# Performance work log

Measured on AMD Instinct MI355X. Metric: run time of the kernel, lower is better.

## Reference

```python
import jax, jax.numpy as jnp
import numpy as np

B, S, I, H = 32, 2048, 256, 256


def setup_inputs() -> dict:
    key = jax.random.key(0)
    ks = jax.random.split(key, 12)
    scale = 1.0 / np.sqrt(H + I)  # torch Linear default init scale-ish
    def w(k):
        return jax.random.normal(k, (H + I, H), dtype=jnp.float32) * scale
    def b(k):
        return jax.random.normal(k, (H,), dtype=jnp.float32) * scale
    return {
        "x": jax.random.normal(ks[0], (B, S, I), dtype=jnp.float32),
        "h0": jax.random.normal(ks[1], (1, B, H), dtype=jnp.float32),
        "c0": jax.random.normal(ks[2], (1, B, H), dtype=jnp.float32),
        "Wf": w(ks[3]), "bf": b(ks[4]),
        "Wi": w(ks[5]), "bi": b(ks[6]),
        "Wc": w(ks[7]), "bc": b(ks[8]),
        "Wo": w(ks[9]), "bo": b(ks[10]),
    }


def reference(x, h0, c0, Wf, bf, Wi, bi, Wc, bc, Wo, bo):
    # Fuse the four gate GEMMs into one: W_all [H+I, 4H], b_all [4H]
    W_all = jnp.concatenate([Wf, Wi, Wc, Wo], axis=1)
    b_all = jnp.concatenate([bf, bi, bc, bo], axis=0)
    Hh = h0.shape[-1]

    def step(carry, x_t):
        h, c = carry  # [B,H]
        hx = jnp.concatenate([h, x_t], axis=-1)          # [B, H+I]
        g = hx @ W_all + b_all                            # [B, 4H]
        f = jax.nn.sigmoid(g[:, 0*Hh:1*Hh])
        i = jax.nn.sigmoid(g[:, 1*Hh:2*Hh])
        cand = jnp.tanh(g[:, 2*Hh:3*Hh])
        o = jax.nn.sigmoid(g[:, 3*Hh:4*Hh])
        c_new = c * f + i * cand
        h_new = o * jnp.tanh(c_new)
        return (h_new, c_new), h_new

    (h_f, c_f), hs = jax.lax.scan(step, (h0[0], c0[0]), jnp.swapaxes(x, 0, 1))
    hidden_states = jnp.swapaxes(hs, 0, 1)               # [B,S,H]
    return hidden_states, (h_f[None], c_f[None])
```

## Files before the change

### kernel.cpp

```cpp
#include <hip/hip_runtime.h>
#include <hip/hip_bf16.h>

typedef __attribute__((ext_vector_type(8))) short short8;
typedef __attribute__((ext_vector_type(4))) float floatx4;
typedef __attribute__((ext_vector_type(4))) unsigned int uintx4;
typedef unsigned int u32;
typedef unsigned long long u64;

#define Bb 32
#define Ss 2048
#define Ii 256
#define Hh 256

#define TAGS_OFF 4096
#define DATA_OFF 8192
#define GX_OFF   65536

#define RETRY_LATCH (1u << 18)
#define RETRY_DEAD  (1u << 22)

__device__ __forceinline__ unsigned short f2bf(float f) {
    unsigned int u = __float_as_uint(f);
    u += 0x7fffu + ((u >> 16) & 1u);
    return (unsigned short)(u >> 16);
}
__device__ __forceinline__ float bf2f_lo(u32 w) { return __uint_as_float(w << 16); }
__device__ __forceinline__ float bf2f_hi(u32 w) { return __uint_as_float(w & 0xffff0000u); }

__device__ __forceinline__ float fast_sigmoid(float x) {
    return __builtin_amdgcn_rcpf(1.0f + __expf(-x));
}
__device__ __forceinline__ float fast_tanh(float x) {
    return 1.0f - 2.0f * __builtin_amdgcn_rcpf(__expf(2.0f * x) + 1.0f);
}

__device__ __forceinline__ void vm_drain() {
    asm volatile("s_waitcnt vmcnt(0)" ::: "memory");
}
__device__ __forceinline__ void tag_load16(const u32* pt, uintx4& a, uintx4& b, uintx4& c, uintx4& d) {
    asm volatile("global_load_dwordx4 %0, %4, off sc0 sc1\n\t"
                 "global_load_dwordx4 %1, %4, off offset:16 sc0 sc1\n\t"
                 "global_load_dwordx4 %2, %4, off offset:32 sc0 sc1\n\t"
                 "global_load_dwordx4 %3, %4, off offset:48 sc0 sc1\n\t"
                 "s_waitcnt vmcnt(0)"
                 : "=v"(a), "=v"(b), "=v"(c), "=v"(d) : "v"(pt) : "memory");
}
__device__ __forceinline__ void data_load8(const u32* pd, uintx4 v[8]) {
    asm volatile("global_load_dwordx4 %0, %8, off sc0 sc1\n\t"
                 "global_load_dwordx4 %1, %8, off offset:64 sc0 sc1\n\t"
                 "global_load_dwordx4 %2, %8, off offset:128 sc0 sc1\n\t"
                 "global_load_dwordx4 %3, %8, off offset:192 sc0 sc1\n\t"
                 "global_load_dwordx4 %4, %8, off offset:256 sc0 sc1\n\t"
                 "global_load_dwordx4 %5, %8, off offset:320 sc0 sc1\n\t"
                 "global_load_dwordx4 %6, %8, off offset:384 sc0 sc1\n\t"
                 "global_load_dwordx4 %7, %8, off offset:448 sc0 sc1\n\t"
                 "s_waitcnt vmcnt(0)"
                 : "=v"(v[0]), "=v"(v[1]), "=v"(v[2]), "=v"(v[3]),
                   "=v"(v[4]), "=v"(v[5]), "=v"(v[6]), "=v"(v[7])
                 : "v"(pd) : "memory");
}

__global__ __launch_bounds__(256, 2)
void lstm_gx_kernel(const float* __restrict__ x,
                    const float* __restrict__ Wf, const float* __restrict__ bfp,
                    const float* __restrict__ Wi, const float* __restrict__ bip,
                    const float* __restrict__ Wc, const float* __restrict__ bcp,
                    const float* __restrict__ Wo, const float* __restrict__ bop,
                    u32* __restrict__ gx)
{
    const int tid = threadIdx.x, wave = tid >> 6, lane = tid & 63;
    const int ln = lane & 15, lg = lane >> 4;
    const int combo = blockIdx.x & 7;
    const int tbase = (blockIdx.x >> 3) * 8;
    const int wg = ((combo & 1) << 2) + wave;
    const int chalf = (combo >> 1) & 1, mtile = combo >> 2;
    const int j0 = wg * 32 + chalf * 16, r0 = mtile * 16;
    const int wv = wg * 4 + chalf * 2 + mtile;

    const float* Wg[4] = {Wf, Wi, Wc, Wo};
    const float* bg[4] = {bfp, bip, bcp, bop};
    float bias[4];
#pragma unroll
    for (int g = 0; g < 4; ++g) bias[g] = bg[g][j0 + ln];

    short8 Bf[4][8];
#pragma unroll
    for (int g = 0; g < 4; ++g)
#pragma unroll
        for (int ks = 0; ks < 8; ++ks) {
            short8 v;
#pragma unroll
            for (int i = 0; i < 8; ++i) {
                int k = 256 + 32 * ks + 8 * lg + i;
                v[i] = (short)f2bf(Wg[g][k * Hh + (j0 + ln)]);
            }
            Bf[g][ks] = v;
        }

    for (int it = 0; it < 8; ++it) {
        int t = tbase + it;
        short8 xf[8];
#pragma unroll
        for (int ks = 0; ks < 8; ++ks) {
            const float* px = x + (r0 + ln) * (Ss * Ii) + t * Ii + 32 * ks + 8 * lg;
            floatx4 a = *(const floatx4*)px;
            floatx4 b = *(const floatx4*)(px + 4);
            short8 v;
#pragma unroll
            for (int q = 0; q < 4; ++q) { v[q] = (short)f2bf(a[q]); v[4 + q] = (short)f2bf(b[q]); }
            xf[ks] = v;
        }
        floatx4 acc[4];
#pragma unroll
        for (int g = 0; g < 4; ++g) acc[g] = (floatx4){0.f, 0.f, 0.f, 0.f};
#pragma unroll
        for (int ks = 0; ks < 8; ++ks)
#pragma unroll
            for (int g = 0; g < 4; ++g)
                acc[g] = __builtin_amdgcn_mfma_f32_16x16x32_bf16(xf[ks], Bf[g][ks], acc[g], 0, 0, 0);

        u32 o[8];
#pragma unroll
        for (int g = 0; g < 4; ++g)
#pragma unroll
            for (int rp = 0; rp < 2; ++rp) {
                float v0 = acc[g][2 * rp] + bias[g];
                float v1 = acc[g][2 * rp + 1] + bias[g];
                o[g * 2 + rp] = (u32)f2bf(v0) | ((u32)f2bf(v1) << 16);
            }
        u32* dst = gx + ((size_t)(t * 32 + wv) * 64 + lane) * 8;
        ((uintx4*)dst)[0] = (uintx4){o[0], o[1], o[2], o[3]};
        ((uintx4*)dst)[1] = (uintx4){o[4], o[5], o[6], o[7]};
    }
}

__global__ __launch_bounds__(256, 1)
void lstm_rec5(const float* __restrict__ h0,
               const float* __restrict__ c0,
               const float* __restrict__ Wf,
               const float* __restrict__ Wi,
               const float* __restrict__ Wc,
               const float* __restrict__ Wo,
               float* __restrict__ out,
               u32* tags, u32* data, const u32* __restrict__ gx)
{
    const int wg = blockIdx.x;
    const int tid = threadIdx.x;
    const int wave = tid >> 6, lane = tid & 63;
    const int mt = wave & 1, chalf = wave >> 1;
    const int ln = lane & 15, lg = lane >> 4;
    const int j0 = wg * 32 + chalf * 16;
    const int j = j0 + ln;
    const int wv = wg * 4 + chalf * 2 + mt;

    const float* Wg[4] = {Wf, Wi, Wc, Wo};
    short8 Bfrag[4][8];
#pragma unroll
    for (int g = 0; g < 4; ++g)
#pragma unroll
        for (int ks = 0; ks < 8; ++ks) {
            short8 v;
#pragma unroll
            for (int i = 0; i < 8; ++i) {
                int k = 32 * ks + 8 * lg + i;
                v[i] = (short)f2bf(Wg[g][k * Hh + j]);
            }
            Bfrag[g][ks] = v;
        }

    float cst[4], hl[4];
#pragma unroll
    for (int r = 0; r < 4; ++r) {
        cst[r] = c0[(16 * mt + 4 * lg + r) * Hh + j];
        hl[r] = 0.0f;
    }

    bool use_atomic = false;

    auto publish = [&](int slot, u32 tag, const float h[4]) {
        u32 wrd[4];
#pragma unroll
        for (int r = 0; r < 4; ++r) {
            float partner = __shfl_xor(h[r], 1);
            wrd[r] = (u32)f2bf(h[r]) | ((u32)f2bf(partner) << 16);
        }
        u32* pd = data + slot * 4096 + (16 * mt + 4 * lg) * 128 + (j >> 1);
        if ((ln & 1) == 0) {
#pragma unroll
            for (int r = 0; r < 4; ++r)
                __hip_atomic_store(pd + 128 * r, wrd[r], __ATOMIC_RELAXED, __HIP_MEMORY_SCOPE_AGENT);
        }
        vm_drain();
        if (lane == 0)
            __hip_atomic_store(tags + (slot * 2 + mt) * 16 + (wg * 2 + chalf), tag,
                               __ATOMIC_RELAXED, __HIP_MEMORY_SCOPE_AGENT);
    };

    {
        float hv0[4];
#pragma unroll
        for (int r = 0; r < 4; ++r) hv0[r] = h0[(16 * mt + 4 * lg + r) * Hh + j];
        publish(0, 1u, hv0);
    }

    uintx4 g0, g1;
    {
        const uintx4* p = (const uintx4*)(gx + ((size_t)wv * 64 + lane) * 8);
        g0 = p[0]; g1 = p[1];
    }

    for (int t = 0; t < Ss; ++t) {
        const int slot = t & 1;
        const u32 want = (u32)(t + 1);
        const u32* pt = tags + (slot * 2 + mt) * 16;

        {
            u32 it = 0;
            for (;;) {
                u32 bad;
                if (!use_atomic) {
                    uintx4 a, b, c, d;
                    tag_load16(pt, a, b, c, d);
                    bad = (a.x ^ want) | (a.y ^ want) | (a.z ^ want) | (a.w ^ want)
                        | (b.x ^ want) | (b.y ^ want) | (b.z ^ want) | (b.w ^ want)
                        | (c.x ^ want) | (c.y ^ want) | (c.z ^ want) | (c.w ^ want)
                        | (d.x ^ want) | (d.y ^ want) | (d.z ^ want) | (d.w ^ want);
                } else {
                    bad = 0;
#pragma unroll
                    for (int i = 0; i < 16; ++i)
                        bad |= __hip_atomic_load(pt + i, __ATOMIC_RELAXED,
                                                 __HIP_MEMORY_SCOPE_AGENT) ^ want;
                }
                if (!__any((int)(bad != 0))) break;
                ++it;
                if (it >= RETRY_LATCH) use_atomic = true;
                if (it >= RETRY_DEAD) break;
            }
        }

        uintx4 dv[8];
        const u32* pd = data + slot * 4096 + (16 * mt + ln) * 128 + 4 * lg;
        if (!use_atomic) {
            data_load8(pd, dv);
        } else {
            const u64* pq = (const u64*)pd;
#pragma unroll
            for (int ks = 0; ks < 8; ++ks) {
                u64 u0 = __hip_atomic_load(pq + 8 * ks,     __ATOMIC_RELAXED, __HIP_MEMORY_SCOPE_AGENT);
                u64 u1 = __hip_atomic_load(pq + 8 * ks + 1, __ATOMIC_RELAXED, __HIP_MEMORY_SCOPE_AGENT);
                dv[ks] = (uintx4){(u32)u0, (u32)(u0 >> 32), (u32)u1, (u32)(u1 >> 32)};
            }
        }

        floatx4 acc[4];
        acc[0] = (floatx4){bf2f_lo(g0.x), bf2f_hi(g0.x), bf2f_lo(g0.y), bf2f_hi(g0.y)};
        acc[1] = (floatx4){bf2f_lo(g0.z), bf2f_hi(g0.z), bf2f_lo(g0.w), bf2f_hi(g0.w)};
        acc[2] = (floatx4){bf2f_lo(g1.x), bf2f_hi(g1.x), bf2f_lo(g1.y), bf2f_hi(g1.y)};
        acc[3] = (floatx4){bf2f_lo(g1.z), bf2f_hi(g1.z), bf2f_lo(g1.w), bf2f_hi(g1.w)};
        if (t + 1 < Ss) {
            const uintx4* pn = (const uintx4*)(gx + ((size_t)((t + 1) * 32 + wv) * 64 + lane) * 8);
            g0 = pn[0]; g1 = pn[1];
        }

#pragma unroll
        for (int ks = 0; ks < 8; ++ks) {
            union { uintx4 u; short8 s; } cv;
            cv.u = dv[ks];
#pragma unroll
            for (int g = 0; g < 4; ++g)
                acc[g] = __builtin_amdgcn_mfma_f32_16x16x32_bf16(cv.s, Bfrag[g][ks], acc[g], 0, 0, 0);
        }

        float hnew[4];
#pragma unroll
        for (int r = 0; r < 4; ++r) {
            float fg = fast_sigmoid(acc[0][r]);
            float ig = fast_sigmoid(acc[1][r]);
            float cd = fast_tanh(acc[2][r]);
            float og = fast_sigmoid(acc[3][r]);
            float c  = cst[r] * fg + ig * cd;
            cst[r] = c;
            hnew[r] = og * fast_tanh(c);
            hl[r] = hnew[r];
        }

        publish((t + 1) & 1, (u32)(t + 2), hnew);
#pragma unroll
        for (int r = 0; r < 4; ++r)
            out[(16 * mt + 4 * lg + r) * (Ss * Hh) + t * Hh + j] = hnew[r];
    }

    float* hfo = out + Bb * Ss * Hh;
    float* cfo = hfo + Bb * Hh;
#pragma unroll
    for (int r = 0; r < 4; ++r) {
        int b = 16 * mt + 4 * lg + r;
        hfo[b * Hh + j] = hl[r];
        cfo[b * Hh + j] = cst[r];
    }
}

extern "C" void kernel_launch(void* const* d_in, const int* in_sizes, int n_in,
                              void* d_out, int out_size, void* d_ws, size_t ws_size,
                              hipStream_t stream) {
    (void)in_sizes; (void)n_in; (void)out_size; (void)ws_size;
    const float* x  = (const float*)d_in[0];
    const float* h0 = (const float*)d_in[1];
    const float* c0 = (const float*)d_in[2];
    const float* Wf = (const float*)d_in[3]; const float* bf = (const float*)d_in[4];
    const float* Wi = (const float*)d_in[5]; const float* bi = (const float*)d_in[6];
    const float* Wc = (const float*)d_in[7]; const float* bc = (const float*)d_in[8];
    const float* Wo = (const float*)d_in[9]; const float* bo = (const float*)d_in[10];

    u32* tags = (u32*)((char*)d_ws + TAGS_OFF);
    u32* data = (u32*)((char*)d_ws + DATA_OFF);
    u32* gx   = (u32*)((char*)d_ws + GX_OFF);


    hipLaunchKernelGGL(lstm_gx_kernel, dim3(2048), dim3(256), 0, stream,
                       x, Wf, bf, Wi, bi, Wc, bc, Wo, bo, gx);
    hipLaunchKernelGGL(lstm_rec5, dim3(8), dim3(256), 0, stream,
                       h0, c0, Wf, Wi, Wc, Wo, (float*)d_out, tags, data, gx);
}
```

Measured before the change: 7.365 ms.

## Replace tag-then-data handoff with self-tagged per-element ring words

```diff
diff --git a/kernel.cpp b/kernel.cpp
--- a/kernel.cpp
+++ b/kernel.cpp
@@ -5,19 +5,16 @@
 typedef __attribute__((ext_vector_type(4))) float floatx4;
 typedef __attribute__((ext_vector_type(4))) unsigned int uintx4;
 typedef unsigned int u32;
-typedef unsigned long long u64;
 
 #define Bb 32
 #define Ss 2048
 #define Ii 256
 #define Hh 256
 
-#define TAGS_OFF 4096
-#define DATA_OFF 8192
-#define GX_OFF   65536
-
-#define RETRY_LATCH (1u << 18)
-#define RETRY_DEAD  (1u << 22)
+#define RING_OFF 8192
+#define GX_OFF   131072
+
+#define RETRY_DEAD (1u << 22)
 
 __device__ __forceinline__ unsigned short f2bf(float f) {
     unsigned int u = __float_as_uint(f);
@@ -34,30 +31,30 @@
     return 1.0f - 2.0f * __builtin_amdgcn_rcpf(__expf(2.0f * x) + 1.0f);
 }
 
-__device__ __forceinline__ void vm_drain() {
-    asm volatile("s_waitcnt vmcnt(0)" ::: "memory");
-}
-__device__ __forceinline__ void tag_load16(const u32* pt, uintx4& a, uintx4& b, uintx4& c, uintx4& d) {
-    asm volatile("global_load_dwordx4 %0, %4, off sc0 sc1\n\t"
-                 "global_load_dwordx4 %1, %4, off offset:16 sc0 sc1\n\t"
-                 "global_load_dwordx4 %2, %4, off offset:32 sc0 sc1\n\t"
-                 "global_load_dwordx4 %3, %4, off offset:48 sc0 sc1\n\t"
-                 "s_waitcnt vmcnt(0)"
-                 : "=v"(a), "=v"(b), "=v"(c), "=v"(d) : "v"(pt) : "memory");
-}
-__device__ __forceinline__ void data_load8(const u32* pd, uintx4 v[8]) {
-    asm volatile("global_load_dwordx4 %0, %8, off sc0 sc1\n\t"
-                 "global_load_dwordx4 %1, %8, off offset:64 sc0 sc1\n\t"
-                 "global_load_dwordx4 %2, %8, off offset:128 sc0 sc1\n\t"
-                 "global_load_dwordx4 %3, %8, off offset:192 sc0 sc1\n\t"
-                 "global_load_dwordx4 %4, %8, off offset:256 sc0 sc1\n\t"
-                 "global_load_dwordx4 %5, %8, off offset:320 sc0 sc1\n\t"
-                 "global_load_dwordx4 %6, %8, off offset:384 sc0 sc1\n\t"
-                 "global_load_dwordx4 %7, %8, off offset:448 sc0 sc1\n\t"
-                 "s_waitcnt vmcnt(0)"
-                 : "=v"(v[0]), "=v"(v[1]), "=v"(v[2]), "=v"(v[3]),
-                   "=v"(v[4]), "=v"(v[5]), "=v"(v[6]), "=v"(v[7])
-                 : "v"(pd) : "memory");
+__device__ __forceinline__ void ring_load_all(const u32* p, uintx4 A[8], uintx4 B[8]) {
+    asm volatile(
+        "global_load_dwordx4 %0, %16, off sc0 sc1\n\t"
+        "global_load_dwordx4 %1, %16, off offset:16 sc0 sc1\n\t"
+        "global_load_dwordx4 %2, %16, off offset:128 sc0 sc1\n\t"
+        "global_load_dwordx4 %3, %16, off offset:144 sc0 sc1\n\t"
+        "global_load_dwordx4 %4, %16, off offset:256 sc0 sc1\n\t"
+        "global_load_dwordx4 %5, %16, off offset:272 sc0 sc1\n\t"
+        "global_load_dwordx4 %6, %16, off offset:384 sc0 sc1\n\t"
+        "global_load_dwordx4 %7, %16, off offset:400 sc0 sc1\n\t"
+        "global_load_dwordx4 %8, %16, off offset:512 sc0 sc1\n\t"
+        "global_load_dwordx4 %9, %16, off offset:528 sc0 sc1\n\t"
+        "global_load_dwordx4 %10, %16, off offset:640 sc0 sc1\n\t"
+        "global_load_dwordx4 %11, %16, off offset:656 sc0 sc1\n\t"
+        "global_load_dwordx4 %12, %16, off offset:768 sc0 sc1\n\t"
+        "global_load_dwordx4 %13, %16, off offset:784 sc0 sc1\n\t"
+        "global_load_dwordx4 %14, %16, off offset:896 sc0 sc1\n\t"
+        "global_load_dwordx4 %15, %16, off offset:912 sc0 sc1\n\t"
+        "s_waitcnt vmcnt(0)"
+        : "=v"(A[0]), "=v"(B[0]), "=v"(A[1]), "=v"(B[1]),
+          "=v"(A[2]), "=v"(B[2]), "=v"(A[3]), "=v"(B[3]),
+          "=v"(A[4]), "=v"(B[4]), "=v"(A[5]), "=v"(B[5]),
+          "=v"(A[6]), "=v"(B[6]), "=v"(A[7]), "=v"(B[7])
+        : "v"(p) : "memory");
 }
 
 __global__ __launch_bounds__(256, 2)
@@ -135,22 +132,21 @@
 }
 
 __global__ __launch_bounds__(256, 1)
-void lstm_rec5(const float* __restrict__ h0,
+void lstm_rec6(const float* __restrict__ h0,
                const float* __restrict__ c0,
                const float* __restrict__ Wf,
                const float* __restrict__ Wi,
                const float* __restrict__ Wc,
                const float* __restrict__ Wo,
                float* __restrict__ out,
-               u32* tags, u32* data, const u32* __restrict__ gx)
+               u32* ring, const u32* __restrict__ gx)
 {
     const int wg = blockIdx.x;
     const int tid = threadIdx.x;
     const int wave = tid >> 6, lane = tid & 63;
     const int mt = wave & 1, chalf = wave >> 1;
     const int ln = lane & 15, lg = lane >> 4;
-    const int j0 = wg * 32 + chalf * 16;
-    const int j = j0 + ln;
+    const int j = wg * 32 + chalf * 16 + ln;
     const int wv = wg * 4 + chalf * 2 + mt;
 
     const float* Wg[4] = {Wf, Wi, Wc, Wo};
@@ -175,32 +171,13 @@
         hl[r] = 0.0f;
     }
 
-    bool use_atomic = false;
-
-    auto publish = [&](int slot, u32 tag, const float h[4]) {
-        u32 wrd[4];
-#pragma unroll
-        for (int r = 0; r < 4; ++r) {
-            float partner = __shfl_xor(h[r], 1);
-            wrd[r] = (u32)f2bf(h[r]) | ((u32)f2bf(partner) << 16);
-        }
-        u32* pd = data + slot * 4096 + (16 * mt + 4 * lg) * 128 + (j >> 1);
-        if ((ln & 1) == 0) {
-#pragma unroll
-            for (int r = 0; r < 4; ++r)
-                __hip_atomic_store(pd + 128 * r, wrd[r], __ATOMIC_RELAXED, __HIP_MEMORY_SCOPE_AGENT);
-        }
-        vm_drain();
-        if (lane == 0)
-            __hip_atomic_store(tags + (slot * 2 + mt) * 16 + (wg * 2 + chalf), tag,
+    {
+        u32* pw = ring + (16 * mt + 4 * lg) * 256 + j;
+#pragma unroll
+        for (int r = 0; r < 4; ++r)
+            __hip_atomic_store(pw + 256 * r,
+                               (1u << 16) | (u32)f2bf(h0[(16 * mt + 4 * lg + r) * Hh + j]),
                                __ATOMIC_RELAXED, __HIP_MEMORY_SCOPE_AGENT);
-    };
-
-    {
-        float hv0[4];
-#pragma unroll
-        for (int r = 0; r < 4; ++r) hv0[r] = h0[(16 * mt + 4 * lg + r) * Hh + j];
-        publish(0, 1u, hv0);
     }
 
     uintx4 g0, g1;
@@ -209,49 +186,11 @@
         g0 = p[0]; g1 = p[1];
     }
 
+    const int myrowbase = (16 * mt + ln) * 256 + 8 * lg;
+
     for (int t = 0; t < Ss; ++t) {
-        const int slot = t & 1;
-        const u32 want = (u32)(t + 1);
-        const u32* pt = tags + (slot * 2 + mt) * 16;
-
-        {
-            u32 it = 0;
-            for (;;) {
-                u32 bad;
-                if (!use_atomic) {
-                    uintx4 a, b, c, d;
-                    tag_load16(pt, a, b, c, d);
-                    bad = (a.x ^ want) | (a.y ^ want) | (a.z ^ want) | (a.w ^ want)
-                        | (b.x ^ want) | (b.y ^ want) | (b.z ^ want) | (b.w ^ want)
-                        | (c.x ^ want) | (c.y ^ want) | (c.z ^ want) | (c.w ^ want)
-                        | (d.x ^ want) | (d.y ^ want) | (d.z ^ want) | (d.w ^ want);
-                } else {
-                    bad = 0;
-#pragma unroll
-                    for (int i = 0; i < 16; ++i)
-                        bad |= __hip_atomic_load(pt + i, __ATOMIC_RELAXED,
-                                                 __HIP_MEMORY_SCOPE_AGENT) ^ want;
-                }
-                if (!__any((int)(bad != 0))) break;
-                ++it;
-                if (it >= RETRY_LATCH) use_atomic = true;
-                if (it >= RETRY_DEAD) break;
-            }
-        }
-
-        uintx4 dv[8];
-        const u32* pd = data + slot * 4096 + (16 * mt + ln) * 128 + 4 * lg;
-        if (!use_atomic) {
-            data_load8(pd, dv);
-        } else {
-            const u64* pq = (const u64*)pd;
-#pragma unroll
-            for (int ks = 0; ks < 8; ++ks) {
-                u64 u0 = __hip_atomic_load(pq + 8 * ks,     __ATOMIC_RELAXED, __HIP_MEMORY_SCOPE_AGENT);
-                u64 u1 = __hip_atomic_load(pq + 8 * ks + 1, __ATOMIC_RELAXED, __HIP_MEMORY_SCOPE_AGENT);
-                dv[ks] = (uintx4){(u32)u0, (u32)(u0 >> 32), (u32)u1, (u32)(u1 >> 32)};
-            }
-        }
+        const u32 want = (u32)(t + 1) << 16;
+        const u32* pd = ring + ((t & 1) ? 8192 : 0) + myrowbase;
 
         floatx4 acc[4];
         acc[0] = (floatx4){bf2f_lo(g0.x), bf2f_hi(g0.x), bf2f_lo(g0.y), bf2f_hi(g0.y)};
@@ -263,14 +202,32 @@
             g0 = pn[0]; g1 = pn[1];
         }
 
-#pragma unroll
-        for (int ks = 0; ks < 8; ++ks) {
-            union { uintx4 u; short8 s; } cv;
-            cv.u = dv[ks];
-#pragma unroll
-            for (int g = 0; g < 4; ++g)
-                acc[g] = __builtin_amdgcn_mfma_f32_16x16x32_bf16(cv.s, Bfrag[g][ks], acc[g], 0, 0, 0);
-        }
+        u32 pend = 0xFFu, it = 0;
+        do {
+            uintx4 A[8], B[8];
+            ring_load_all(pd, A, B);
+#pragma unroll
+            for (int ks = 0; ks < 8; ++ks) {
+                if (pend & (1u << ks)) {
+                    u32 bad = ((A[ks].x ^ want) | (A[ks].y ^ want) |
+                               (A[ks].z ^ want) | (A[ks].w ^ want) |
+                               (B[ks].x ^ want) | (B[ks].y ^ want) |
+                               (B[ks].z ^ want) | (B[ks].w ^ want)) & 0xFFFF0000u;
+                    if (!__any((int)(bad != 0))) {
+                        union { u32 u[4]; short8 s; } f;
+                        f.u[0] = __builtin_amdgcn_perm(A[ks].y, A[ks].x, 0x05040100u);
+                        f.u[1] = __builtin_amdgcn_perm(A[ks].w, A[ks].z, 0x05040100u);
+                        f.u[2] = __builtin_amdgcn_perm(B[ks].y, B[ks].x, 0x05040100u);
+                        f.u[3] = __builtin_amdgcn_perm(B[ks].w, B[ks].z, 0x05040100u);
+#pragma unroll
+                        for (int g = 0; g < 4; ++g)
+                            acc[g] = __builtin_amdgcn_mfma_f32_16x16x32_bf16(f.s, Bfrag[g][ks], acc[g], 0, 0, 0);
+                        pend &= ~(1u << ks);
+                    }
+                }
+            }
+            if (++it >= RETRY_DEAD) break;
+        } while (pend);
 
         float hnew[4];
 #pragma unroll
@@ -285,7 +242,14 @@
             hl[r] = hnew[r];
         }
 
-        publish((t + 1) & 1, (u32)(t + 2), hnew);
+        {
+            const u32 ntag = (u32)(t + 2) << 16;
+            u32* pw = ring + (((t + 1) & 1) ? 8192 : 0) + (16 * mt + 4 * lg) * 256 + j;
+#pragma unroll
+            for (int r = 0; r < 4; ++r)
+                __hip_atomic_store(pw + 256 * r, ntag | (u32)f2bf(hnew[r]),
+                                   __ATOMIC_RELAXED, __HIP_MEMORY_SCOPE_AGENT);
+        }
 #pragma unroll
         for (int r = 0; r < 4; ++r)
             out[(16 * mt + 4 * lg + r) * (Ss * Hh) + t * Hh + j] = hnew[r];
@@ -313,13 +277,12 @@
     const float* Wc = (const float*)d_in[7]; const float* bc = (const float*)d_in[8];
     const float* Wo = (const float*)d_in[9]; const float* bo = (const float*)d_in[10];
 
-    u32* tags = (u32*)((char*)d_ws + TAGS_OFF);
-    u32* data = (u32*)((char*)d_ws + DATA_OFF);
+    u32* ring = (u32*)((char*)d_ws + RING_OFF);
     u32* gx   = (u32*)((char*)d_ws + GX_OFF);
 
 
     hipLaunchKernelGGL(lstm_gx_kernel, dim3(2048), dim3(256), 0, stream,
                        x, Wf, bf, Wi, bi, Wc, bc, Wo, bo, gx);
-    hipLaunchKernelGGL(lstm_rec5, dim3(8), dim3(256), 0, stream,
-                       h0, c0, Wf, Wi, Wc, Wo, (float*)d_out, tags, data, gx);
-}
+    hipLaunchKernelGGL(lstm_rec6, dim3(8), dim3(256), 0, stream,
+                       h0, c0, Wf, Wi, Wc, Wo, (float*)d_out, ring, gx);
+}
```

New measurement: 9.060 ms. 23.0% more time.
